# Kernel tuning notes

Measured on AMD Instinct MI355X. Metric: run time of the kernel, lower is better.

The kernel has to match this reference:

```python
import jax, jax.numpy as jnp
import numpy as np

P, Q, B = 1024, 128, 64
HP, HQ, A = 1024, 1024, 75

def setup_inputs() -> dict:
    key = jax.random.key(0)
    ks = jax.random.split(key, 10)
    def w(k, shape, fan_in):
        return jax.random.uniform(k, shape, jnp.float32, -1.0, 1.0) / np.sqrt(fan_in)
    return {
        "h_passage": jax.random.normal(ks[0], (P, B, HP), jnp.float32),
        "u_question": jax.random.normal(ks[1], (Q, B, HQ), jnp.float32),
        "Whp": w(ks[2], (A, HP), HP),
        "Wha": w(ks[3], (A, HQ), HQ),
        "v_w": w(ks[4], (1, A), A),
        "Wuq": w(ks[5], (A, HQ), HQ),
        "v1_w": w(ks[6], (1, A), A),
        "v1_b": w(ks[7], (1,), A),
        "W_ih": w(ks[8], (3 * HQ, HP), HQ),  # GRUCell input->hidden, no bias
        "W_hh": w(ks[9], (3 * HQ, HQ), HQ),  # GRUCell hidden->hidden, no bias
    }

def gru_cell(x, h, W_ih, W_hh):
    # torch GRUCell (bias=False): gates ordered [r, z, n]
    gi = x @ W_ih.T            # (B, 3H)
    gh = h @ W_hh.T            # (B, 3H)
    i_r, i_z, i_n = jnp.split(gi, 3, axis=-1)
    h_r, h_z, h_n = jnp.split(gh, 3, axis=-1)
    r = jax.nn.sigmoid(i_r + h_r)
    z = jax.nn.sigmoid(i_z + h_z)
    n = jnp.tanh(i_n + r * h_n)
    return (1.0 - z) * n + z * h

def reference(h_passage, u_question, Whp, Wha, v_w, Wuq, v1_w, v1_b, W_ih, W_hh):
    # initial state: additive attention pooling over the question (axis 0)
    s = jnp.tanh(u_question @ Wuq.T) @ v1_w.T + v1_b      # (Q, B, 1)
    a = jax.nn.softmax(s, axis=0)
    ha0 = jnp.sum(a * u_question, axis=0)                 # (B, HQ)

    Wh = h_passage @ Whp.T                                # (P, B, A)

    s1 = jnp.tanh(Wh + ha0 @ Wha.T) @ v_w.T               # (P, B, 1)
    start_logits = jnp.transpose(s1, (1, 0, 2))           # (B, P, 1)
    a1 = jax.nn.softmax(s1, axis=0)
    c = jnp.sum(a1 * h_passage, axis=0)                   # (B, HP)
    ha1 = gru_cell(c, ha0, W_ih, W_hh)                    # (B, HQ)

    s2 = jnp.tanh(Wh + ha1 @ Wha.T) @ v_w.T               # (P, B, 1)
    end_logits = jnp.transpose(s2, (1, 0, 2))             # (B, P, 1)
    return (start_logits, end_logits)
```

## Files before the change

kernel.cpp:

```cpp
#include <hip/hip_runtime.h>
#include <math.h>

#define PP 1024
#define QQ 128
#define BB 64
#define HH 1024
#define AA 75
#define APAD 80
#define H3 3072
#define BM 128
#define BK 32
#define NTILE 32
#define LDA 40

#define OFF_SQ    0L
#define OFF_AQ    8192L
#define OFF_HA0   16384L
#define OFF_HAW0  81920L
#define OFF_WH    87040L
#define OFF_S1    5329920L
#define OFF_A1    5395456L
#define OFF_C     5460992L
#define OFF_GI    5526528L
#define OFF_GH    5723136L
#define OFF_HA1   5919744L
#define OFF_HAW1  5985280L

typedef __attribute__((ext_vector_type(8))) __bf16 bf16x8;
typedef __attribute__((ext_vector_type(8))) unsigned short ushort8;
typedef __attribute__((ext_vector_type(4))) float f32x4;

__device__ __forceinline__ unsigned short f2bf(float x) {
    unsigned int u = __builtin_bit_cast(unsigned int, x);
    u += 0x7FFFu + ((u >> 16) & 1u);
    return (unsigned short)(u >> 16);
}
__device__ __forceinline__ float bf2f(unsigned short h) {
    unsigned int u = ((unsigned int)h) << 16;
    return __builtin_bit_cast(float, u);
}
__device__ __forceinline__ f32x4 mfma16(ushort8 a, ushort8 b, f32x4 c) {
    return __builtin_amdgcn_mfma_f32_16x16x32_bf16(
        __builtin_bit_cast(bf16x8, a), __builtin_bit_cast(bf16x8, b), c, 0, 0, 0);
}
__device__ __forceinline__ void cvt_hilo4(const float4 x, ushort4& h, ushort4& lo) {
    __bf16 a = (__bf16)x.x, b = (__bf16)x.y, c = (__bf16)x.z, d = (__bf16)x.w;
    h.x = __builtin_bit_cast(unsigned short, a);
    h.y = __builtin_bit_cast(unsigned short, b);
    h.z = __builtin_bit_cast(unsigned short, c);
    h.w = __builtin_bit_cast(unsigned short, d);
    lo.x = __builtin_bit_cast(unsigned short, (__bf16)(x.x - (float)a));
    lo.y = __builtin_bit_cast(unsigned short, (__bf16)(x.y - (float)b));
    lo.z = __builtin_bit_cast(unsigned short, (__bf16)(x.z - (float)c));
    lo.w = __builtin_bit_cast(unsigned short, (__bf16)(x.w - (float)d));
}
__device__ __forceinline__ void gl2lds16(const void* g, void* s) {
    __builtin_amdgcn_global_load_lds(
        (const __attribute__((address_space(1))) unsigned int*)g,
        (__attribute__((address_space(3))) unsigned int*)s, 16, 0, 0);
}
__device__ __forceinline__ void split_store(unsigned short* hi, unsigned short* lo,
                                            int idx, float4 x) {
    ushort4 h, l;
    cvt_hilo4(x, h, l);
    *reinterpret_cast<ushort4*>(hi + idx) = h;
    *reinterpret_cast<ushort4*>(lo + idx) = l;
}

__global__ __launch_bounds__(256) void split_w(const float* __restrict__ Wsrc,
                                               unsigned short* __restrict__ dst) {
    const int n = blockIdx.x * 256 + threadIdx.x;
    const int a = n % 80;
    const int kg = (n / 80) & 3;
    const int hl = (n / 320) & 1;
    const int tile = n / 640;
    const int k = tile * 32 + kg * 8;
    float4 x0 = make_float4(0.f, 0.f, 0.f, 0.f), x1 = x0;
    if (a < AA) {
        x0 = *reinterpret_cast<const float4*>(Wsrc + (size_t)a * 1024 + k);
        x1 = *reinterpret_cast<const float4*>(Wsrc + (size_t)a * 1024 + k + 4);
    }
    ushort4 h0, l0, h1, l1;
    cvt_hilo4(x0, h0, l0);
    cvt_hilo4(x1, h1, l1);
    ushort8 o;
    if (hl == 0) { o[0]=h0.x; o[1]=h0.y; o[2]=h0.z; o[3]=h0.w; o[4]=h1.x; o[5]=h1.y; o[6]=h1.z; o[7]=h1.w; }
    else         { o[0]=l0.x; o[1]=l0.y; o[2]=l0.z; o[3]=l0.w; o[4]=l1.x; o[5]=l1.y; o[6]=l1.z; o[7]=l1.w; }
    *reinterpret_cast<ushort8*>(dst + (size_t)n * 8) = o;
}

template <bool ADD_HAW, bool STORE_RAW, bool ADD_BIAS>
__global__ __launch_bounds__(256) void gemm_attn(
    const float* __restrict__ X,
    const unsigned short* __restrict__ Wsp,
    const float* __restrict__ haW,
    const float* __restrict__ vw,
    const float* __restrict__ bias,
    float* __restrict__ raw_out,
    float* __restrict__ s_out)
{
    __shared__ __align__(16) float X32[2][BM][BK];
    __shared__ __align__(16) unsigned short Xbf[2][4][BM][8];
    __shared__ __align__(16) unsigned short Bsh[3][5120];

    const int t = threadIdx.x;
    const int w = t >> 6;
    const int l = t & 63;
    const int lr = l & 15;
    const int lg = l >> 4;
    const int l3 = l >> 3;
    const int l7 = l & 7;
    const int row0 = blockIdx.x * BM;

    float vwv[5];
#pragma unroll
    for (int nt = 0; nt < 5; nt++) {
        const int col = lr + 16 * nt;
        vwv[nt] = (col < AA) ? vw[col] : 0.f;
    }
    asm volatile("s_waitcnt vmcnt(0)" ::: "memory");

    f32x4 acc[2][5];
#pragma unroll
    for (int mt = 0; mt < 2; mt++)
#pragma unroll
        for (int nt = 0; nt < 5; nt++) acc[mt][nt] = (f32x4){0.f, 0.f, 0.f, 0.f};

    const int swz = (l7 ^ l3);

#define ISSUE_X(tile, buf)                                                      \
    {                                                                           \
        _Pragma("unroll")                                                       \
        for (int c = 0; c < 4; c++) {                                           \
            const int r = w * 32 + c * 8 + l3;                                  \
            const float* src = X + (size_t)(row0 + r) * 1024 + (tile) * BK + swz * 4; \
            gl2lds16(src, &X32[buf][w * 32 + c * 8][0]);                        \
        }                                                                       \
    }
#define ISSUE_B(tile, bufb)                                                     \
    {                                                                           \
        _Pragma("unroll")                                                       \
        for (int j = 0; j < 3; j++) {                                           \
            int cc = w * 3 + j;                                                 \
            if (cc >= 10) cc -= 10;                 \
            const unsigned short* src = Wsp + (size_t)(tile) * 5120 + cc * 512 + l * 8; \
            gl2lds16(src, &Bsh[bufb][cc * 512]);                                \
        }                                                                       \
    }

    ISSUE_X(0, 0);
    ISSUE_B(0, 0);

    for (int tt = 0; tt < NTILE; ++tt) {
        const int cur = tt & 1;
        const int bufB = tt % 3;
        if (tt + 1 < NTILE) {
            ISSUE_X(tt + 1, cur ^ 1);
            ISSUE_B(tt + 1, (tt + 1) % 3);
            asm volatile("s_waitcnt vmcnt(7)" ::: "memory");
        } else {
            asm volatile("s_waitcnt vmcnt(0)" ::: "memory");
        }
        __builtin_amdgcn_sched_barrier(0);

#pragma unroll
        for (int i = 0; i < 4; i++) {
            const int r = w * 32 + i * 8 + l3;
            const float4 x = *reinterpret_cast<const float4*>(&X32[cur][r][swz * 4]);
            ushort4 h, lo;
            cvt_hilo4(x, h, lo);
            const int kg = l7 >> 1, hf = (l7 & 1) * 4;
            *reinterpret_cast<ushort4*>(&Xbf[0][kg][r][hf]) = h;
            *reinterpret_cast<ushort4*>(&Xbf[1][kg][r][hf]) = lo;
        }

        asm volatile("s_barrier" ::: "memory");

        ushort8 ah0h, ah0l, ah1h, ah1l;
        ah0h = *reinterpret_cast<const ushort8*>(&Xbf[0][lg][w * 32 + 0 + lr][0]);
        ah0l = *reinterpret_cast<const ushort8*>(&Xbf[1][lg][w * 32 + 0 + lr][0]);
        ah1h = *reinterpret_cast<const ushort8*>(&Xbf[0][lg][w * 32 + 16 + lr][0]);
        ah1l = *reinterpret_cast<const ushort8*>(&Xbf[1][lg][w * 32 + 16 + lr][0]);
#pragma unroll
        for (int nt = 0; nt < 5; nt++) {
            const int aoff = lg * 640 + (nt * 16 + lr) * 8;
            const ushort8 bh = *reinterpret_cast<const ushort8*>(&Bsh[bufB][aoff]);
            const ushort8 bl = *reinterpret_cast<const ushort8*>(&Bsh[bufB][2560 + aoff]);
            acc[0][nt] = mfma16(ah0h, bh, acc[0][nt]);
            acc[0][nt] = mfma16(ah0h, bl, acc[0][nt]);
            acc[0][nt] = mfma16(ah0l, bh, acc[0][nt]);
            acc[1][nt] = mfma16(ah1h, bh, acc[1][nt]);
            acc[1][nt] = mfma16(ah1h, bl, acc[1][nt]);
            acc[1][nt] = mfma16(ah1l, bh, acc[1][nt]);
        }
    }
#undef ISSUE_X
#undef ISSUE_B

#pragma unroll
    for (int mt = 0; mt < 2; mt++) {
#pragma unroll
        for (int r = 0; r < 4; r++) {
            const int row_local = w * 32 + mt * 16 + lg * 4 + r;
            const int rg = row0 + row_local;
            const int b = rg & 63;
            float partial = 0.f;
#pragma unroll
            for (int nt = 0; nt < 5; nt++) {
                const int col = lr + 16 * nt;
                const float v = acc[mt][nt][r];
                if (STORE_RAW) raw_out[(size_t)rg * APAD + col] = v;
                if (col < AA) {
                    float hw = 0.f;
                    if (ADD_HAW) hw = haW[b * APAD + col];
                    partial += vwv[nt] * tanhf(v + hw);
                }
            }
            partial += __shfl_xor(partial, 1);
            partial += __shfl_xor(partial, 2);
            partial += __shfl_xor(partial, 4);
            partial += __shfl_xor(partial, 8);
            if (lr == 0) {
                if (ADD_BIAS) partial += bias[0];
                s_out[rg] = partial;
            }
        }
    }
}

__global__ __launch_bounds__(128) void softmax_q(const float* __restrict__ sq,
                                                 float* __restrict__ aq) {
    const int b = blockIdx.x;
    const int q = threadIdx.x;
    __shared__ float red[2], red2[2];
    float v = sq[q * BB + b];
    float m = v;
#pragma unroll
    for (int off = 1; off < 64; off <<= 1) m = fmaxf(m, __shfl_xor(m, off));
    if ((q & 63) == 0) red[q >> 6] = m;
    __syncthreads();
    m = fmaxf(red[0], red[1]);
    float e = expf(v - m);
    float s = e;
#pragma unroll
    for (int off = 1; off < 64; off <<= 1) s += __shfl_xor(s, off);
    if ((q & 63) == 0) red2[q >> 6] = s;
    __syncthreads();
    s = red2[0] + red2[1];
    aq[q * BB + b] = e / s;
}

__global__ __launch_bounds__(256) void pool_q(const float* __restrict__ u,
                                              const float* __restrict__ aq,
                                              float* __restrict__ ha0) {
    const int b = blockIdx.y;
    const int h = blockIdx.x * 256 + threadIdx.x;
    __shared__ float aw[QQ];
    if (threadIdx.x < QQ) aw[threadIdx.x] = aq[threadIdx.x * BB + b];
    __syncthreads();
    float acc = 0.f;
#pragma unroll 4
    for (int q = 0; q < QQ; q++)
        acc += aw[q] * u[(q * BB + b) * HH + h];
    ha0[b * HH + h] = acc;
}

__global__ __launch_bounds__(64) void vecmat(const float* __restrict__ x,
                                             const float* __restrict__ W,
                                             float* __restrict__ out) {
    const int a = blockIdx.x, b = blockIdx.y, l = threadIdx.x;
    float s = 0.f;
#pragma unroll 4
    for (int k = l; k < HH; k += 64) s += x[b * HH + k] * W[a * HH + k];
#pragma unroll
    for (int off = 1; off < 64; off <<= 1) s += __shfl_xor(s, off);
    if (l == 0) out[b * APAD + a] = s;
}

__global__ __launch_bounds__(256) void softmax_p(const float* __restrict__ s1,
                                                 float* __restrict__ a1,
                                                 float* __restrict__ outStart) {
    const int b = blockIdx.x;
    const int t = threadIdx.x;
    __shared__ float r4[4], r4b[4];
    float v[4];
    float m = -1e30f;
#pragma unroll
    for (int i = 0; i < 4; i++) {
        const int p = t + i * 256;
        v[i] = s1[p * BB + b];
        outStart[b * PP + p] = v[i];
        m = fmaxf(m, v[i]);
    }
#pragma unroll
    for (int off = 1; off < 64; off <<= 1) m = fmaxf(m, __shfl_xor(m, off));
    if ((t & 63) == 0) r4[t >> 6] = m;
    __syncthreads();
    m = fmaxf(fmaxf(r4[0], r4[1]), fmaxf(r4[2], r4[3]));
    float e[4];
    float s = 0.f;
#pragma unroll
    for (int i = 0; i < 4; i++) {
        e[i] = expf(v[i] - m);
        s += e[i];
    }
#pragma unroll
    for (int off = 1; off < 64; off <<= 1) s += __shfl_xor(s, off);
    if ((t & 63) == 0) r4b[t >> 6] = s;
    __syncthreads();
    s = r4b[0] + r4b[1] + r4b[2] + r4b[3];
    const float inv = 1.f / s;
#pragma unroll
    for (int i = 0; i < 4; i++) a1[(t + i * 256) * BB + b] = e[i] * inv;
}

__global__ __launch_bounds__(256) void weighted_pool_p(
    const float* __restrict__ hp, const float* __restrict__ a1,
    float* __restrict__ c) {
    const int b = blockIdx.y;
    const int h = blockIdx.x * 256 + threadIdx.x;
    const int ps = blockIdx.z;
    __shared__ float aw[128];
    if (threadIdx.x < 128) aw[threadIdx.x] = a1[(ps * 128 + threadIdx.x) * BB + b];
    __syncthreads();
    float acc = 0.f;
    const long base = ((long)ps * 128 * BB + b) * HH + h;
#pragma unroll 4
    for (int p = 0; p < 128; p++)
        acc += aw[p] * hp[base + (long)p * (BB * HH)];
    atomicAdd(&c[b * HH + h], acc);
}

__global__ __launch_bounds__(256) void gru_gemm(
    const float* __restrict__ c, const float* __restrict__ ha0,
    const float* __restrict__ W_ih, const float* __restrict__ W_hh,
    float* __restrict__ gi, float* __restrict__ gh) {
    const float* X = blockIdx.y ? ha0 : c;
    const float* W = blockIdx.y ? W_hh : W_ih;
    float* out = blockIdx.y ? gh : gi;
    const int n0 = blockIdx.x * 64;

    __shared__ unsigned short Ah[64 * LDA], Al[64 * LDA];
    __shared__ unsigned short Bh[64 * LDA], Bl[64 * LDA];

    const int t = threadIdx.x;
    const int w = t >> 6;
    const int l = t & 63;
    const int lr = l & 15;
    const int lg = l >> 4;

    f32x4 acc[4];
#pragma unroll
    for (int mt = 0; mt < 4; mt++) acc[mt] = (f32x4){0.f, 0.f, 0.f, 0.f};

    for (int k0 = 0; k0 < 1024; k0 += 32) {
        __syncthreads();
#pragma unroll
        for (int i = 0; i < 2; i++) {
            const int s = t + i * 256;
            const int row = s >> 3, kq = s & 7;
            const float4 x = *reinterpret_cast<const float4*>(
                X + (size_t)row * 1024 + k0 + kq * 4);
            split_store(Ah, Al, row * LDA + kq * 4, x);
            const float4 wv = *reinterpret_cast<const float4*>(
                W + (size_t)(n0 + row) * 1024 + k0 + kq * 4);
            split_store(Bh, Bl, row * LDA + kq * 4, wv);
        }
        __syncthreads();

        const int br = (w * 16 + lr) * LDA + lg * 8;
        const ushort8 bh = *reinterpret_cast<const ushort8*>(&Bh[br]);
        const ushort8 bl = *reinterpret_cast<const ushort8*>(&Bl[br]);
#pragma unroll
        for (int mt = 0; mt < 4; mt++) {
            const int ar = (mt * 16 + lr) * LDA + lg * 8;
            const ushort8 ah = *reinterpret_cast<const ushort8*>(&Ah[ar]);
            const ushort8 al = *reinterpret_cast<const ushort8*>(&Al[ar]);
            acc[mt] = mfma16(ah, bh, acc[mt]);
            acc[mt] = mfma16(ah, bl, acc[mt]);
            acc[mt] = mfma16(al, bh, acc[mt]);
        }
    }

#pragma unroll
    for (int mt = 0; mt < 4; mt++)
#pragma unroll
        for (int r = 0; r < 4; r++) {
            const int row = mt * 16 + lg * 4 + r;
            const int n = n0 + w * 16 + lr;
            out[(size_t)row * H3 + n] = acc[mt][r];
        }
}

__global__ __launch_bounds__(256) void gru_gate(const float* __restrict__ gi,
                                                const float* __restrict__ gh,
                                                const float* __restrict__ ha0,
                                                float* __restrict__ ha1) {
    const int b = blockIdx.y;
    const int hn = blockIdx.x * 256 + threadIdx.x;
    const long o = (long)b * H3 + hn;
    const float r = 1.f / (1.f + expf(-(gi[o] + gh[o])));
    const float z = 1.f / (1.f + expf(-(gi[o + 1024] + gh[o + 1024])));
    const float n = tanhf(gi[o + 2048] + r * gh[o + 2048]);
    ha1[b * HH + hn] = (1.f - z) * n + z * ha0[b * HH + hn];
}

__global__ __launch_bounds__(256) void end_logits_k(
    const float* __restrict__ wh, const float* __restrict__ haW1,
    const float* __restrict__ vw, float* __restrict__ out) {
    const int row0 = blockIdx.x * 64;
    const int t = threadIdx.x;
    const int l = t & 15;
    const int rbase = (t >> 4) * 4;
#pragma unroll
    for (int i = 0; i < 4; i++) {
        const int r = row0 + rbase + i;
        const int b = r & 63;
        float partial = 0.f;
#pragma unroll
        for (int j = 0; j < 5; j++) {
            const int col = l + 16 * j;
            if (col < AA)
                partial +=
                    vw[col] * tanhf(wh[(size_t)r * APAD + col] + haW1[b * APAD + col]);
        }
        partial += __shfl_xor(partial, 1);
        partial += __shfl_xor(partial, 2);
        partial += __shfl_xor(partial, 4);
        partial += __shfl_xor(partial, 8);
        if (l == 0) {
            const int p = r >> 6;
            out[(size_t)BB * PP + b * PP + p] = partial;
        }
    }
}

extern "C" void kernel_launch(void* const* d_in, const int* in_sizes, int n_in,
                              void* d_out, int out_size, void* d_ws,
                              size_t ws_size, hipStream_t stream) {
    const float* hp   = (const float*)d_in[0];
    const float* u    = (const float*)d_in[1];
    const float* Whp  = (const float*)d_in[2];
    const float* Wha  = (const float*)d_in[3];
    const float* v_w  = (const float*)d_in[4];
    const float* Wuq  = (const float*)d_in[5];
    const float* v1w  = (const float*)d_in[6];
    const float* v1b  = (const float*)d_in[7];
    const float* W_ih = (const float*)d_in[8];
    const float* W_hh = (const float*)d_in[9];
    float* out = (float*)d_out;
    float* ws = (float*)d_ws;
    unsigned short* wsp_hp = (unsigned short*)(ws + OFF_GI);
    unsigned short* wsp_uq = (unsigned short*)(ws + OFF_GH);

    hipLaunchKernelGGL(split_w, dim3(80), dim3(256), 0, stream, Whp, wsp_hp);
    hipLaunchKernelGGL(split_w, dim3(80), dim3(256), 0, stream, Wuq, wsp_uq);
    hipLaunchKernelGGL((gemm_attn<false, false, true>), dim3(QQ * BB / BM),
                       dim3(256), 0, stream, u, wsp_uq, nullptr, v1w, v1b,
                       nullptr, ws + OFF_SQ);
    hipLaunchKernelGGL(softmax_q, dim3(BB), dim3(128), 0, stream, ws + OFF_SQ,
                       ws + OFF_AQ);
    hipLaunchKernelGGL(pool_q, dim3(HH / 256, BB), dim3(256), 0, stream, u,
                       ws + OFF_AQ, ws + OFF_HA0);
    hipLaunchKernelGGL(vecmat, dim3(AA, BB), dim3(64), 0, stream, ws + OFF_HA0,
                       Wha, ws + OFF_HAW0);
    hipLaunchKernelGGL((gemm_attn<true, true, false>), dim3(PP * BB / BM),
                       dim3(256), 0, stream, hp, wsp_hp, ws + OFF_HAW0, v_w,
                       nullptr, ws + OFF_WH, ws + OFF_S1);
    hipLaunchKernelGGL(softmax_p, dim3(BB), dim3(256), 0, stream, ws + OFF_S1,
                       ws + OFF_A1, out);
    hipMemsetAsync(ws + OFF_C, 0, (size_t)BB * HH * sizeof(float), stream);
    hipLaunchKernelGGL(weighted_pool_p, dim3(HH / 256, BB, 8), dim3(256), 0,
                       stream, hp, ws + OFF_A1, ws + OFF_C);
    hipLaunchKernelGGL(gru_gemm, dim3(H3 / 64, 2), dim3(256), 0, stream,
                       ws + OFF_C, ws + OFF_HA0, W_ih, W_hh, ws + OFF_GI,
                       ws + OFF_GH);
    hipLaunchKernelGGL(gru_gate, dim3(HH / 256, BB), dim3(256), 0, stream,
                       ws + OFF_GI, ws + OFF_GH, ws + OFF_HA0, ws + OFF_HA1);
    hipLaunchKernelGGL(vecmat, dim3(AA, BB), dim3(64), 0, stream, ws + OFF_HA1,
                       Wha, ws + OFF_HAW1);
    hipLaunchKernelGGL(end_logits_k, dim3(PP * BB / 64), dim3(256), 0, stream,
                       ws + OFF_WH, ws + OFF_HAW1, v_w, out);
    (void)in_sizes; (void)n_in; (void)out_size; (void)ws_size;
}
```

Baseline: 624.2 us.

## Register-prefetch X in attention GEMM, fuse init/gate kernels, transpose score layout

The attention GEMM stops staging fp32 X through LDS with async loads. Each thread instead prefetches X two tiles ahead into registers, uses a 4-deep B ring, and unrolls the loop by two. The question softmax, pooling and Wha projection are fused into one init_state kernel, and the GRU gate is fused with the second Wha projection. Score arrays are stored batch-major so the softmax and pooling reads are contiguous. gru_gemm gets register prefetch of the next K tile. The cost targeted is LDS traffic and launch count, in exchange for higher register pressure and fewer, larger per-batch blocks in the fused kernels.

```diff
diff --git a/kernel.cpp b/kernel.cpp
--- a/kernel.cpp
+++ b/kernel.cpp
@@ -30,15 +30,6 @@
 typedef __attribute__((ext_vector_type(8))) unsigned short ushort8;
 typedef __attribute__((ext_vector_type(4))) float f32x4;
 
-__device__ __forceinline__ unsigned short f2bf(float x) {
-    unsigned int u = __builtin_bit_cast(unsigned int, x);
-    u += 0x7FFFu + ((u >> 16) & 1u);
-    return (unsigned short)(u >> 16);
-}
-__device__ __forceinline__ float bf2f(unsigned short h) {
-    unsigned int u = ((unsigned int)h) << 16;
-    return __builtin_bit_cast(float, u);
-}
 __device__ __forceinline__ f32x4 mfma16(ushort8 a, ushort8 b, f32x4 c) {
     return __builtin_amdgcn_mfma_f32_16x16x32_bf16(
         __builtin_bit_cast(bf16x8, a), __builtin_bit_cast(bf16x8, b), c, 0, 0, 0);
@@ -97,19 +88,16 @@
     const float* __restrict__ vw,
     const float* __restrict__ bias,
     float* __restrict__ raw_out,
-    float* __restrict__ s_out)
+    float* __restrict__ s_out,
+    const int sstr)
 {
-    __shared__ __align__(16) float X32[2][BM][BK];
     __shared__ __align__(16) unsigned short Xbf[2][4][BM][8];
-    __shared__ __align__(16) unsigned short Bsh[3][5120];
+    __shared__ __align__(16) unsigned short Bsh[4][5120];
 
     const int t = threadIdx.x;
-    const int w = t >> 6;
-    const int l = t & 63;
-    const int lr = l & 15;
-    const int lg = l >> 4;
-    const int l3 = l >> 3;
-    const int l7 = l & 7;
+    const int w = t >> 6, l = t & 63;
+    const int lr = l & 15, lg = l >> 4;
+    const int l3 = l >> 3, l7 = l & 7;
     const int row0 = blockIdx.x * BM;
 
     float vwv[5];
@@ -118,7 +106,6 @@
         const int col = lr + 16 * nt;
         vwv[nt] = (col < AA) ? vw[col] : 0.f;
     }
-    asm volatile("s_waitcnt vmcnt(0)" ::: "memory");
 
     f32x4 acc[2][5];
 #pragma unroll
@@ -126,83 +113,85 @@
 #pragma unroll
         for (int nt = 0; nt < 5; nt++) acc[mt][nt] = (f32x4){0.f, 0.f, 0.f, 0.f};
 
-    const int swz = (l7 ^ l3);
-
-#define ISSUE_X(tile, buf)                                                      \
-    {                                                                           \
-        _Pragma("unroll")                                                       \
-        for (int c = 0; c < 4; c++) {                                           \
-            const int r = w * 32 + c * 8 + l3;                                  \
-            const float* src = X + (size_t)(row0 + r) * 1024 + (tile) * BK + swz * 4; \
-            gl2lds16(src, &X32[buf][w * 32 + c * 8][0]);                        \
-        }                                                                       \
-    }
-#define ISSUE_B(tile, bufb)                                                     \
+    const float* xbase = X + (size_t)(row0 + w * 32 + l3) * 1024 + l7 * 4;
+
+#define SB __builtin_amdgcn_sched_barrier(0)
+#define BAR asm volatile("s_barrier" ::: "memory")
+#define ISSUE_B(tile)                                                           \
     {                                                                           \
         _Pragma("unroll")                                                       \
         for (int j = 0; j < 3; j++) {                                           \
             int cc = w * 3 + j;                                                 \
-            if (cc >= 10) cc -= 10;                 \
-            const unsigned short* src = Wsp + (size_t)(tile) * 5120 + cc * 512 + l * 8; \
-            gl2lds16(src, &Bsh[bufb][cc * 512]);                                \
+            if (cc >= 10) cc -= 10;     \
+            gl2lds16(Wsp + (size_t)(tile) * 5120 + cc * 512 + l * 8,            \
+                     &Bsh[(tile) & 3][cc * 512]);                               \
         }                                                                       \
     }
-
-    ISSUE_X(0, 0);
-    ISSUE_B(0, 0);
-
-    for (int tt = 0; tt < NTILE; ++tt) {
-        const int cur = tt & 1;
-        const int bufB = tt % 3;
-        if (tt + 1 < NTILE) {
-            ISSUE_X(tt + 1, cur ^ 1);
-            ISSUE_B(tt + 1, (tt + 1) % 3);
-            asm volatile("s_waitcnt vmcnt(7)" ::: "memory");
-        } else {
-            asm volatile("s_waitcnt vmcnt(0)" ::: "memory");
-        }
-        __builtin_amdgcn_sched_barrier(0);
-
-#pragma unroll
-        for (int i = 0; i < 4; i++) {
-            const int r = w * 32 + i * 8 + l3;
-            const float4 x = *reinterpret_cast<const float4*>(&X32[cur][r][swz * 4]);
-            ushort4 h, lo;
-            cvt_hilo4(x, h, lo);
-            const int kg = l7 >> 1, hf = (l7 & 1) * 4;
-            *reinterpret_cast<ushort4*>(&Xbf[0][kg][r][hf]) = h;
-            *reinterpret_cast<ushort4*>(&Xbf[1][kg][r][hf]) = lo;
-        }
-
-        asm volatile("s_barrier" ::: "memory");
-
-        ushort8 ah0h, ah0l, ah1h, ah1l;
-        ah0h = *reinterpret_cast<const ushort8*>(&Xbf[0][lg][w * 32 + 0 + lr][0]);
-        ah0l = *reinterpret_cast<const ushort8*>(&Xbf[1][lg][w * 32 + 0 + lr][0]);
-        ah1h = *reinterpret_cast<const ushort8*>(&Xbf[0][lg][w * 32 + 16 + lr][0]);
-        ah1l = *reinterpret_cast<const ushort8*>(&Xbf[1][lg][w * 32 + 16 + lr][0]);
-#pragma unroll
-        for (int nt = 0; nt < 5; nt++) {
-            const int aoff = lg * 640 + (nt * 16 + lr) * 8;
-            const ushort8 bh = *reinterpret_cast<const ushort8*>(&Bsh[bufB][aoff]);
-            const ushort8 bl = *reinterpret_cast<const ushort8*>(&Bsh[bufB][2560 + aoff]);
-            acc[0][nt] = mfma16(ah0h, bh, acc[0][nt]);
-            acc[0][nt] = mfma16(ah0h, bl, acc[0][nt]);
-            acc[0][nt] = mfma16(ah0l, bh, acc[0][nt]);
-            acc[1][nt] = mfma16(ah1h, bh, acc[1][nt]);
-            acc[1][nt] = mfma16(ah1h, bl, acc[1][nt]);
-            acc[1][nt] = mfma16(ah1l, bh, acc[1][nt]);
-        }
-    }
-#undef ISSUE_X
+#define LOADX(tile, v0, v1, v2, v3)                                             \
+    {                                                                           \
+        const float* p_ = xbase + (tile) * BK;                                  \
+        v0 = *reinterpret_cast<const float4*>(p_);                              \
+        v1 = *reinterpret_cast<const float4*>(p_ + 8 * 1024);                   \
+        v2 = *reinterpret_cast<const float4*>(p_ + 16 * 1024);                  \
+        v3 = *reinterpret_cast<const float4*>(p_ + 24 * 1024);                  \
+    }
+#define CVT1(vv, c)                                                             \
+    {                                                                           \
+        ushort4 h_, lo_;                                                        \
+        cvt_hilo4(vv, h_, lo_);                                                 \
+        const int r_ = w * 32 + (c) * 8 + l3;                                   \
+        *reinterpret_cast<ushort4*>(&Xbf[0][l7 >> 1][r_][(l7 & 1) * 4]) = h_;   \
+        *reinterpret_cast<ushort4*>(&Xbf[1][l7 >> 1][r_][(l7 & 1) * 4]) = lo_;  \
+    }
+#define MFMA_PHASE(buf)                                                         \
+    {                                                                           \
+        const unsigned short* Bp = &Bsh[(buf)][0];                              \
+        const ushort8 ah0h = *reinterpret_cast<const ushort8*>(&Xbf[0][lg][w * 32 + lr][0]);      \
+        const ushort8 ah0l = *reinterpret_cast<const ushort8*>(&Xbf[1][lg][w * 32 + lr][0]);      \
+        const ushort8 ah1h = *reinterpret_cast<const ushort8*>(&Xbf[0][lg][w * 32 + 16 + lr][0]); \
+        const ushort8 ah1l = *reinterpret_cast<const ushort8*>(&Xbf[1][lg][w * 32 + 16 + lr][0]); \
+        _Pragma("unroll")                                                       \
+        for (int nt = 0; nt < 5; nt++) {                                        \
+            const int aoff = lg * 640 + (nt * 16 + lr) * 8;                     \
+            const ushort8 bh = *reinterpret_cast<const ushort8*>(&Bp[aoff]);    \
+            const ushort8 bl = *reinterpret_cast<const ushort8*>(&Bp[2560 + aoff]); \
+            acc[0][nt] = mfma16(ah0h, bh, acc[0][nt]);                          \
+            acc[0][nt] = mfma16(ah0h, bl, acc[0][nt]);                          \
+            acc[0][nt] = mfma16(ah0l, bh, acc[0][nt]);                          \
+            acc[1][nt] = mfma16(ah1h, bh, acc[1][nt]);                          \
+            acc[1][nt] = mfma16(ah1h, bl, acc[1][nt]);                          \
+            acc[1][nt] = mfma16(ah1l, bh, acc[1][nt]);                          \
+        }                                                                       \
+    }
+
+    float4 a0, a1, a2, a3, b0, b1, b2, b3;
+    ISSUE_B(0); SB;
+    LOADX(0, a0, a1, a2, a3); SB;
+    ISSUE_B(1); SB;
+    LOADX(1, b0, b1, b2, b3); SB;
+
+    for (int tt = 0; tt < NTILE; tt += 2) {
+        CVT1(a0, 0); CVT1(a1, 1); CVT1(a2, 2); CVT1(a3, 3);
+        if (tt + 2 < NTILE) { ISSUE_B(tt + 2); SB; LOADX(tt + 2, a0, a1, a2, a3); SB; }
+        BAR;
+        MFMA_PHASE(tt & 3);
+        CVT1(b0, 0); CVT1(b1, 1); CVT1(b2, 2); CVT1(b3, 3);
+        if (tt + 3 < NTILE) { ISSUE_B(tt + 3); SB; LOADX(tt + 3, b0, b1, b2, b3); SB; }
+        BAR;
+        MFMA_PHASE((tt + 1) & 3);
+    }
+#undef SB
+#undef BAR
 #undef ISSUE_B
+#undef LOADX
+#undef CVT1
+#undef MFMA_PHASE
 
 #pragma unroll
     for (int mt = 0; mt < 2; mt++) {
 #pragma unroll
         for (int r = 0; r < 4; r++) {
-            const int row_local = w * 32 + mt * 16 + lg * 4 + r;
-            const int rg = row0 + row_local;
+            const int rg = row0 + w * 32 + mt * 16 + lg * 4 + r;
             const int b = rg & 63;
             float partial = 0.f;
 #pragma unroll
@@ -222,59 +211,56 @@
             partial += __shfl_xor(partial, 8);
             if (lr == 0) {
                 if (ADD_BIAS) partial += bias[0];
-                s_out[rg] = partial;
+                s_out[(size_t)b * sstr + (rg >> 6)] = partial;
             }
         }
     }
 }
 
-__global__ __launch_bounds__(128) void softmax_q(const float* __restrict__ sq,
-                                                 float* __restrict__ aq) {
+__global__ __launch_bounds__(512) void init_state(
+    const float* __restrict__ u, const float* __restrict__ sq,
+    const float* __restrict__ Wha, float* __restrict__ ha0,
+    float* __restrict__ haW0) {
     const int b = blockIdx.x;
-    const int q = threadIdx.x;
-    __shared__ float red[2], red2[2];
-    float v = sq[q * BB + b];
-    float m = v;
-#pragma unroll
-    for (int off = 1; off < 64; off <<= 1) m = fmaxf(m, __shfl_xor(m, off));
-    if ((q & 63) == 0) red[q >> 6] = m;
-    __syncthreads();
-    m = fmaxf(red[0], red[1]);
-    float e = expf(v - m);
-    float s = e;
-#pragma unroll
-    for (int off = 1; off < 64; off <<= 1) s += __shfl_xor(s, off);
-    if ((q & 63) == 0) red2[q >> 6] = s;
-    __syncthreads();
-    s = red2[0] + red2[1];
-    aq[q * BB + b] = e / s;
-}
-
-__global__ __launch_bounds__(256) void pool_q(const float* __restrict__ u,
-                                              const float* __restrict__ aq,
-                                              float* __restrict__ ha0) {
-    const int b = blockIdx.y;
-    const int h = blockIdx.x * 256 + threadIdx.x;
+    const int t = threadIdx.x;
     __shared__ float aw[QQ];
-    if (threadIdx.x < QQ) aw[threadIdx.x] = aq[threadIdx.x * BB + b];
-    __syncthreads();
-    float acc = 0.f;
+    __shared__ float ha0s[HH];
+    if (t < QQ) aw[t] = sq[b * QQ + t];
+    __syncthreads();
+    if (t < 64) {
+        float m = fmaxf(aw[t], aw[t + 64]);
+#pragma unroll
+        for (int off = 1; off < 64; off <<= 1) m = fmaxf(m, __shfl_xor(m, off));
+        const float e0 = expf(aw[t] - m), e1 = expf(aw[t + 64] - m);
+        float s = e0 + e1;
+#pragma unroll
+        for (int off = 1; off < 64; off <<= 1) s += __shfl_xor(s, off);
+        const float inv = 1.f / s;
+        aw[t] = e0 * inv;
+        aw[t + 64] = e1 * inv;
+    }
+    __syncthreads();
+#pragma unroll
+    for (int j = 0; j < 2; j++) {
+        const int h = t + j * 512;
+        float acc = 0.f;
 #pragma unroll 4
-    for (int q = 0; q < QQ; q++)
-        acc += aw[q] * u[(q * BB + b) * HH + h];
-    ha0[b * HH + h] = acc;
-}
-
-__global__ __launch_bounds__(64) void vecmat(const float* __restrict__ x,
-                                             const float* __restrict__ W,
-                                             float* __restrict__ out) {
-    const int a = blockIdx.x, b = blockIdx.y, l = threadIdx.x;
-    float s = 0.f;
-#pragma unroll 4
-    for (int k = l; k < HH; k += 64) s += x[b * HH + k] * W[a * HH + k];
-#pragma unroll
-    for (int off = 1; off < 64; off <<= 1) s += __shfl_xor(s, off);
-    if (l == 0) out[b * APAD + a] = s;
+        for (int q = 0; q < QQ; q++)
+            acc += aw[q] * u[(size_t)(q * BB + b) * HH + h];
+        ha0s[h] = acc;
+        ha0[b * HH + h] = acc;
+    }
+    __syncthreads();
+    const int w8 = t >> 6, l = t & 63;
+    for (int a = w8; a < AA; a += 8) {
+        float s = 0.f;
+#pragma unroll
+        for (int j = 0; j < 16; j++)
+            s += ha0s[l + 64 * j] * Wha[(size_t)a * HH + l + 64 * j];
+#pragma unroll
+        for (int off = 1; off < 64; off <<= 1) s += __shfl_xor(s, off);
+        if (l == 0) haW0[b * APAD + a] = s;
+    }
 }
 
 __global__ __launch_bounds__(256) void softmax_p(const float* __restrict__ s1,
@@ -288,7 +274,7 @@
 #pragma unroll
     for (int i = 0; i < 4; i++) {
         const int p = t + i * 256;
-        v[i] = s1[p * BB + b];
+        v[i] = s1[b * PP + p];
         outStart[b * PP + p] = v[i];
         m = fmaxf(m, v[i]);
     }
@@ -311,7 +297,7 @@
     s = r4b[0] + r4b[1] + r4b[2] + r4b[3];
     const float inv = 1.f / s;
 #pragma unroll
-    for (int i = 0; i < 4; i++) a1[(t + i * 256) * BB + b] = e[i] * inv;
+    for (int i = 0; i < 4; i++) a1[b * PP + t + i * 256] = e[i] * inv;
 }
 
 __global__ __launch_bounds__(256) void weighted_pool_p(
@@ -321,11 +307,11 @@
     const int h = blockIdx.x * 256 + threadIdx.x;
     const int ps = blockIdx.z;
     __shared__ float aw[128];
-    if (threadIdx.x < 128) aw[threadIdx.x] = a1[(ps * 128 + threadIdx.x) * BB + b];
+    if (threadIdx.x < 128) aw[threadIdx.x] = a1[b * PP + ps * 128 + threadIdx.x];
     __syncthreads();
     float acc = 0.f;
     const long base = ((long)ps * 128 * BB + b) * HH + h;
-#pragma unroll 4
+#pragma unroll 8
     for (int p = 0; p < 128; p++)
         acc += aw[p] * hp[base + (long)p * (BB * HH)];
     atomicAdd(&c[b * HH + h], acc);
@@ -348,23 +334,31 @@
     const int l = t & 63;
     const int lr = l & 15;
     const int lg = l >> 4;
+    const int r0 = t >> 3, q0 = t & 7;
+    const int r1 = (t + 256) >> 3, q1 = t & 7;
 
     f32x4 acc[4];
 #pragma unroll
     for (int mt = 0; mt < 4; mt++) acc[mt] = (f32x4){0.f, 0.f, 0.f, 0.f};
+
+    float4 xc0 = *reinterpret_cast<const float4*>(X + (size_t)r0 * 1024 + q0 * 4);
+    float4 xc1 = *reinterpret_cast<const float4*>(X + (size_t)r1 * 1024 + q1 * 4);
+    float4 wc0 = *reinterpret_cast<const float4*>(W + (size_t)(n0 + r0) * 1024 + q0 * 4);
+    float4 wc1 = *reinterpret_cast<const float4*>(W + (size_t)(n0 + r1) * 1024 + q1 * 4);
 
     for (int k0 = 0; k0 < 1024; k0 += 32) {
         __syncthreads();
-#pragma unroll
-        for (int i = 0; i < 2; i++) {
-            const int s = t + i * 256;
-            const int row = s >> 3, kq = s & 7;
-            const float4 x = *reinterpret_cast<const float4*>(
-                X + (size_t)row * 1024 + k0 + kq * 4);
-            split_store(Ah, Al, row * LDA + kq * 4, x);
-            const float4 wv = *reinterpret_cast<const float4*>(
-                W + (size_t)(n0 + row) * 1024 + k0 + kq * 4);
-            split_store(Bh, Bl, row * LDA + kq * 4, wv);
+        split_store(Ah, Al, r0 * LDA + q0 * 4, xc0);
+        split_store(Ah, Al, r1 * LDA + q1 * 4, xc1);
+        split_store(Bh, Bl, r0 * LDA + q0 * 4, wc0);
+        split_store(Bh, Bl, r1 * LDA + q1 * 4, wc1);
+        float4 xn0 = xc0, xn1 = xc1, wn0 = wc0, wn1 = wc1;
+        if (k0 + 32 < 1024) {
+            const int kk = k0 + 32;
+            xn0 = *reinterpret_cast<const float4*>(X + (size_t)r0 * 1024 + kk + q0 * 4);
+            xn1 = *reinterpret_cast<const float4*>(X + (size_t)r1 * 1024 + kk + q1 * 4);
+            wn0 = *reinterpret_cast<const float4*>(W + (size_t)(n0 + r0) * 1024 + kk + q0 * 4);
+            wn1 = *reinterpret_cast<const float4*>(W + (size_t)(n0 + r1) * 1024 + kk + q1 * 4);
         }
         __syncthreads();
 
@@ -380,6 +374,7 @@
             acc[mt] = mfma16(ah, bl, acc[mt]);
             acc[mt] = mfma16(al, bh, acc[mt]);
         }
+        xc0 = xn0; xc1 = xn1; wc0 = wn0; wc1 = wn1;
     }
 
 #pragma unroll
@@ -392,17 +387,32 @@
         }
 }
 
-__global__ __launch_bounds__(256) void gru_gate(const float* __restrict__ gi,
-                                                const float* __restrict__ gh,
-                                                const float* __restrict__ ha0,
-                                                float* __restrict__ ha1) {
-    const int b = blockIdx.y;
-    const int hn = blockIdx.x * 256 + threadIdx.x;
-    const long o = (long)b * H3 + hn;
-    const float r = 1.f / (1.f + expf(-(gi[o] + gh[o])));
-    const float z = 1.f / (1.f + expf(-(gi[o + 1024] + gh[o + 1024])));
-    const float n = tanhf(gi[o + 2048] + r * gh[o + 2048]);
-    ha1[b * HH + hn] = (1.f - z) * n + z * ha0[b * HH + hn];
+__global__ __launch_bounds__(512) void gate_haw(
+    const float* __restrict__ gi, const float* __restrict__ gh,
+    const float* __restrict__ ha0, const float* __restrict__ Wha,
+    float* __restrict__ haW1) {
+    const int b = blockIdx.x, t = threadIdx.x;
+    __shared__ float hs[HH];
+#pragma unroll
+    for (int j = 0; j < 2; j++) {
+        const int hn = t + j * 512;
+        const size_t o = (size_t)b * H3 + hn;
+        const float r = 1.f / (1.f + expf(-(gi[o] + gh[o])));
+        const float z = 1.f / (1.f + expf(-(gi[o + 1024] + gh[o + 1024])));
+        const float n = tanhf(gi[o + 2048] + r * gh[o + 2048]);
+        hs[hn] = (1.f - z) * n + z * ha0[b * HH + hn];
+    }
+    __syncthreads();
+    const int w8 = t >> 6, l = t & 63;
+    for (int a = w8; a < AA; a += 8) {
+        float s = 0.f;
+#pragma unroll
+        for (int j = 0; j < 16; j++)
+            s += hs[l + 64 * j] * Wha[(size_t)a * HH + l + 64 * j];
+#pragma unroll
+        for (int off = 1; off < 64; off <<= 1) s += __shfl_xor(s, off);
+        if (l == 0) haW1[b * APAD + a] = s;
+    }
 }
 
 __global__ __launch_bounds__(256) void end_logits_k(
@@ -457,16 +467,12 @@
     hipLaunchKernelGGL(split_w, dim3(80), dim3(256), 0, stream, Wuq, wsp_uq);
     hipLaunchKernelGGL((gemm_attn<false, false, true>), dim3(QQ * BB / BM),
                        dim3(256), 0, stream, u, wsp_uq, nullptr, v1w, v1b,
-                       nullptr, ws + OFF_SQ);
-    hipLaunchKernelGGL(softmax_q, dim3(BB), dim3(128), 0, stream, ws + OFF_SQ,
-                       ws + OFF_AQ);
-    hipLaunchKernelGGL(pool_q, dim3(HH / 256, BB), dim3(256), 0, stream, u,
-                       ws + OFF_AQ, ws + OFF_HA0);
-    hipLaunchKernelGGL(vecmat, dim3(AA, BB), dim3(64), 0, stream, ws + OFF_HA0,
-                       Wha, ws + OFF_HAW0);
+                       nullptr, ws + OFF_SQ, QQ);
+    hipLaunchKernelGGL(init_state, dim3(BB), dim3(512), 0, stream, u,
+                       ws + OFF_SQ, Wha, ws + OFF_HA0, ws + OFF_HAW0);
     hipLaunchKernelGGL((gemm_attn<true, true, false>), dim3(PP * BB / BM),
                        dim3(256), 0, stream, hp, wsp_hp, ws + OFF_HAW0, v_w,
-                       nullptr, ws + OFF_WH, ws + OFF_S1);
+                       nullptr, ws + OFF_WH, ws + OFF_S1, PP);
     hipLaunchKernelGGL(softmax_p, dim3(BB), dim3(256), 0, stream, ws + OFF_S1,
                        ws + OFF_A1, out);
     hipMemsetAsync(ws + OFF_C, 0, (size_t)BB * HH * sizeof(float), stream);
@@ -475,10 +481,8 @@
     hipLaunchKernelGGL(gru_gemm, dim3(H3 / 64, 2), dim3(256), 0, stream,
                        ws + OFF_C, ws + OFF_HA0, W_ih, W_hh, ws + OFF_GI,
                        ws + OFF_GH);
-    hipLaunchKernelGGL(gru_gate, dim3(HH / 256, BB), dim3(256), 0, stream,
-                       ws + OFF_GI, ws + OFF_GH, ws + OFF_HA0, ws + OFF_HA1);
-    hipLaunchKernelGGL(vecmat, dim3(AA, BB), dim3(64), 0, stream, ws + OFF_HA1,
-                       Wha, ws + OFF_HAW1);
+    hipLaunchKernelGGL(gate_haw, dim3(BB), dim3(512), 0, stream, ws + OFF_GI,
+                       ws + OFF_GH, ws + OFF_HA0, Wha, ws + OFF_HAW1);
     hipLaunchKernelGGL(end_logits_k, dim3(PP * BB / 64), dim3(256), 0, stream,
                        ws + OFF_WH, ws + OFF_HAW1, v_w, out);
     (void)in_sizes; (void)n_in; (void)out_size; (void)ws_size;
```

Result: faster. 607.5 us (-2.7%).
